# Optimization experiments

Measured on AMD Instinct MI355X. Metric: run time of the kernel, lower is better.

The kernel has to match this reference:

```python
import jax, jax.numpy as jnp
import numpy as np

N_NODES = 500_000
N_EDGES = 8_000_000
N_GRAPHS = 1000


def _mlp(x, w1, b1, w2, b2):
    # Linear -> SELU -> Linear (torch Sequential equivalent)
    return jax.nn.selu(x @ w1 + b1) @ w2 + b2


def setup_inputs() -> dict:
    key = jax.random.key(0)
    ks = jax.random.split(key, 25)
    p = lambda i, shape: jax.random.normal(ks[i], shape, jnp.float32) * 0.1
    return {
        "nodes": jax.random.normal(ks[0], (N_NODES, 1), jnp.float32),
        "edges": jax.random.normal(ks[1], (N_EDGES, 1), jnp.float32),
        "senders": jax.random.randint(ks[2], (N_EDGES,), 0, N_NODES),
        "receivers": jax.random.randint(ks[3], (N_EDGES,), 0, N_NODES),
        "graph_ids": jnp.sort(jax.random.randint(ks[4], (N_NODES,), 0, N_GRAPHS)),
        "num_graphs": N_GRAPHS,
        # permutate_nodes: 2 -> 10 -> 10
        "pn_w1": p(5, (2, 10)), "pn_b1": p(6, (10,)), "pn_w2": p(7, (10, 10)), "pn_b2": p(8, (10,)),
        # update_edges: 11 -> 5 -> 1
        "ue_w1": p(9, (11, 5)), "ue_b1": p(10, (5,)), "ue_w2": p(11, (5, 1)), "ue_b2": p(12, (1,)),
        # permutate_edges: 1 -> 5 -> 10
        "pe_w1": p(13, (1, 5)), "pe_b1": p(14, (5,)), "pe_w2": p(15, (5, 10)), "pe_b2": p(16, (10,)),
        # update_nodes: 11 -> 5 -> 1
        "un_w1": p(17, (11, 5)), "un_b1": p(18, (5,)), "un_w2": p(19, (5, 1)), "un_b2": p(20, (1,)),
        # predict: 11 -> 10 -> 10
        "pr_w1": p(21, (11, 10)), "pr_b1": p(22, (10,)), "pr_w2": p(23, (10, 10)), "pr_b2": p(24, (10,)),
    }


def reference(nodes, edges, pn_w1, pn_b1, pn_w2, pn_b2,
              ue_w1, ue_b1, ue_w2, ue_b2,
              pe_w1, pe_b1, pe_w2, pe_b2,
              un_w1, un_b1, un_w2, un_b2,
              pr_w1, pr_b1, pr_w2, pr_b2,
              senders, receivers, graph_ids, num_graphs):
    # gather node feats to edges: [recv || send] -> (E, 2)
    collected = jnp.concatenate([nodes[receivers], nodes[senders]], axis=-1)
    h1_nodes = _mlp(collected, pn_w1, pn_b1, pn_w2, pn_b2)  # (E, 10)
    h1_edges = edges  # (E, 1)
    for _ in range(3):
        h1_edges = _mlp(jnp.concatenate([h1_edges, h1_nodes], axis=-1),
                        ue_w1, ue_b1, ue_w2, ue_b2)  # (E, 1)
    # edges -> nodes aggregation (sum over receiver)
    edges_of_nodes = jax.ops.segment_sum(h1_edges, receivers, num_segments=nodes.shape[0])  # (N, 1)
    h2_edges = _mlp(edges_of_nodes, pe_w1, pe_b1, pe_w2, pe_b2)  # (N, 10)
    h2_nodes = nodes  # (N, 1)
    for _ in range(3):
        h2_nodes = _mlp(jnp.concatenate([h2_nodes, h2_edges], axis=-1),
                        un_w1, un_b1, un_w2, un_b2)  # (N, 1)
    # nodes -> globals aggregation (sum per graph)
    g = jax.ops.segment_sum(jnp.concatenate([h2_nodes, h2_edges], axis=-1),
                            graph_ids, num_segments=num_graphs)  # (G, 11)
    out = _mlp(g, pr_w1, pr_b1, pr_w2, pr_b2)  # (G, 10)
    return jax.nn.softmax(out, axis=-1)
```

## Files before the change

kernel.cpp:

```cpp
#include <hip/hip_runtime.h>
#include <hip/hip_fp16.h>
#include <math.h>

#define N_NODES_C  500000
#define N_EDGES_C  8000000
#define N_GRAPHS_C 1000
#define NGROUPS_C  (N_EDGES_C / 4)

#define BSHIFT  11
#define BWIDTH  2048
#define NBKT    245

#define PART_TPB 512
#define EPB     16384
#define GPB     (EPB / 4)
#define NPB     ((NGROUPS_C + GPB - 1) / GPB)
#define SROW    496
#define RITER   (GPB / PART_TPB)

#define GRAPH_ACC_OFF 0
#define PARTIALS_OFF  11008
#define FW_OFF        33024
#define STARTS_OFF    33280
#define PAIRS_OFF     (STARTS_OFF + 246 * SROW)
#define WS_WORDS_NEEDED (PAIRS_OFF + NPB * EPB)
#define ZERO_HEAD     33024
#define OLD_NODE_ACC_OFF 33536
#define OLD_ZERO_WORDS   (OLD_NODE_ACC_OFF + N_NODES_C)

#define LOG2E_F 1.4426950408889634f


__device__ __forceinline__ float selu2(float xl) {
    const float C1 = 0.7282901039f;
    const float C2 = 1.7580993408473766f;
    float e = __builtin_amdgcn_exp2f(xl);
    float neg = fmaf(C2, e, -C2);
    return xl > 0.0f ? C1 * xl : neg;
}

__device__ __forceinline__ float selu_f(float x) {
    const float scale = 1.0507009873554805f;
    const float sa    = 1.0507009873554805f * 1.6732632423543772f;
    float neg = sa * (__expf(x) - 1.0f);
    return x > 0.0f ? scale * x : neg;
}

__device__ __forceinline__ void atomAddF(float* p, float v) {
    __hip_atomic_fetch_add(p, v, __ATOMIC_RELAXED, __HIP_MEMORY_SCOPE_AGENT);
}

__device__ __forceinline__ void fuse_weights(
        int t,
        const float* __restrict__ pn_w1, const float* __restrict__ pn_b1,
        const float* __restrict__ pn_w2, const float* __restrict__ pn_b2,
        const float* __restrict__ ue_w1, const float* __restrict__ ue_b1,
        const float* __restrict__ ue_w2, const float* __restrict__ ue_b2,
        const float* __restrict__ pe_w1, const float* __restrict__ pe_b1,
        const float* __restrict__ pe_w2, const float* __restrict__ pe_b2,
        const float* __restrict__ un_w1, const float* __restrict__ un_b1,
        const float* __restrict__ un_w2, const float* __restrict__ un_b2,
        float* __restrict__ fw) {
    const float L = LOG2E_F;
    if (t < 20) fw[0 + t] = pn_w1[t] * L;
    if (t < 10) fw[20 + t] = pn_b1[t] * L;
    if (t < 50) {
        int j = t / 5, k = t % 5;
        float s = 0.0f;
        for (int m = 0; m < 10; ++m) s += pn_w2[j * 10 + m] * ue_w1[(1 + m) * 5 + k];
        fw[30 + t] = s * L;
    }
    if (t < 5) {
        float s = ue_b1[t];
        for (int m = 0; m < 10; ++m) s += pn_b2[m] * ue_w1[(1 + m) * 5 + t];
        fw[80 + t] = s * L;
    }
    if (t < 5)  fw[85 + t]  = ue_w1[t] * L;
    if (t < 5)  fw[90 + t]  = ue_w2[t];
    if (t == 0) fw[95]      = ue_b2[0];
    if (t < 5)  fw[96 + t]  = pe_w1[t] * L;
    if (t < 5)  fw[101 + t] = pe_b1[t] * L;
    if (t < 50) fw[106 + t] = pe_w2[t];
    if (t < 10) fw[156 + t] = pe_b2[t];
    if (t < 25) {
        int j = t / 5, k = t % 5;
        float s = 0.0f;
        for (int m = 0; m < 10; ++m) s += pe_w2[j * 10 + m] * un_w1[(1 + m) * 5 + k];
        fw[166 + t] = s * L;
    }
    if (t < 5) {
        float s = un_b1[t];
        for (int m = 0; m < 10; ++m) s += pe_b2[m] * un_w1[(1 + m) * 5 + t];
        fw[191 + t] = s * L;
    }
    if (t < 5)  fw[196 + t] = un_w1[t] * L;
    if (t < 5)  fw[201 + t] = un_w2[t];
    if (t == 0) fw[206]     = un_b2[0];
}

__global__ __launch_bounds__(256) void k_init(
        float* __restrict__ ws,
        const float* pn_w1, const float* pn_b1, const float* pn_w2, const float* pn_b2,
        const float* ue_w1, const float* ue_b1, const float* ue_w2, const float* ue_b2,
        const float* pe_w1, const float* pe_b1, const float* pe_w2, const float* pe_b2,
        const float* un_w1, const float* un_b1, const float* un_w2, const float* un_b2) {
    int i = blockIdx.x * 256 + threadIdx.x;
    if (i < ZERO_HEAD) ws[i] = 0.0f;
    if (blockIdx.x == 0)
        fuse_weights(threadIdx.x, pn_w1, pn_b1, pn_w2, pn_b2, ue_w1, ue_b1, ue_w2, ue_b2,
                     pe_w1, pe_b1, pe_w2, pe_b2, un_w1, un_b1, un_w2, un_b2, ws + FW_OFF);
}

__global__ void k_fuse(const float* pn_w1, const float* pn_b1, const float* pn_w2, const float* pn_b2,
                       const float* ue_w1, const float* ue_b1, const float* ue_w2, const float* ue_b2,
                       const float* pe_w1, const float* pe_b1, const float* pe_w2, const float* pe_b2,
                       const float* un_w1, const float* un_b1, const float* un_w2, const float* un_b2,
                       float* fw) {
    fuse_weights(threadIdx.x, pn_w1, pn_b1, pn_w2, pn_b2, ue_w1, ue_b1, ue_w2, ue_b2,
                 pe_w1, pe_b1, pe_w2, pe_b2, un_w1, un_b1, un_w2, un_b2, fw);
}

__global__ void k_final(const float* __restrict__ graph_acc,
                        const float* __restrict__ partials,
                        const float* __restrict__ pr_w1, const float* __restrict__ pr_b1,
                        const float* __restrict__ pr_w2, const float* __restrict__ pr_b2,
                        float* __restrict__ out) {
    int g = blockIdx.x * blockDim.x + threadIdx.x;
    if (g >= N_GRAPHS_C) return;
    float gv[11];
#pragma unroll
    for (int f = 0; f < 11; ++f)
        gv[f] = graph_acc[g * 11 + f] + partials[g * 11 + f] + partials[11000 + g * 11 + f];
    float h[10];
#pragma unroll
    for (int j = 0; j < 10; ++j) {
        float z = pr_b1[j];
#pragma unroll
        for (int f = 0; f < 11; ++f) z = fmaf(gv[f], pr_w1[f * 10 + j], z);
        h[j] = selu_f(z);
    }
    float o[10];
    float mx = -1e30f;
#pragma unroll
    for (int j = 0; j < 10; ++j) {
        float z = pr_b2[j];
#pragma unroll
        for (int m = 0; m < 10; ++m) z = fmaf(h[m], pr_w2[m * 10 + j], z);
        o[j] = z;
        mx = fmaxf(mx, z);
    }
    float sum = 0.0f;
#pragma unroll
    for (int j = 0; j < 10; ++j) { o[j] = __expf(o[j] - mx); sum += o[j]; }
    float inv = 1.0f / sum;
#pragma unroll
    for (int j = 0; j < 10; ++j) out[g * 10 + j] = o[j] * inv;
}


__global__ __launch_bounds__(PART_TPB, 4) void k_part(
        const float* __restrict__ nodes, const float* __restrict__ edges,
        const int* __restrict__ senders, const int* __restrict__ receivers,
        const float* __restrict__ fw, int* __restrict__ starts_T,
        unsigned int* __restrict__ pairs) {
    __shared__ int hist[256];
    __shared__ int cursorS[256];
    __shared__ unsigned int staged[EPB];

    int tid = threadIdx.x;
    int p   = blockIdx.x;
    int gstart = p * GPB;
    int gnum   = NGROUPS_C - gstart;
    if (gnum > GPB) gnum = GPB;

    float w_pn1[20], b_pn1[10], W_eb[50], b_eb[5], w1r0[5], w2e[5];
#pragma unroll
    for (int j = 0; j < 20; ++j) w_pn1[j] = fw[j];
#pragma unroll
    for (int j = 0; j < 10; ++j) b_pn1[j] = fw[20 + j];
#pragma unroll
    for (int j = 0; j < 50; ++j) W_eb[j] = fw[30 + j];
#pragma unroll
    for (int j = 0; j < 5; ++j) b_eb[j] = fw[80 + j];
#pragma unroll
    for (int j = 0; j < 5; ++j) w1r0[j] = fw[85 + j];
#pragma unroll
    for (int j = 0; j < 5; ++j) w2e[j] = fw[90 + j];
    float b2e = fw[95];

    if (tid < 256) hist[tid] = 0;
    __syncthreads();

    int4 rv4[RITER];
#pragma unroll
    for (int r = 0; r < RITER; ++r) {
        int idx = r * PART_TPB + tid;
        int gi  = gstart + (idx < gnum ? idx : 0);
        rv4[r] = ((const int4*)receivers)[gi];
        if (idx < gnum) {
            atomicAdd(&hist[rv4[r].x >> BSHIFT], 1);
            atomicAdd(&hist[rv4[r].y >> BSHIFT], 1);
            atomicAdd(&hist[rv4[r].z >> BSHIFT], 1);
            atomicAdd(&hist[rv4[r].w >> BSHIFT], 1);
        }
    }
    __syncthreads();

    int orig = 0, val = 0;
    if (tid < 256) { orig = hist[tid]; val = orig; }
    for (int d = 1; d < 256; d <<= 1) {
        int add = 0;
        if (tid >= d && tid < 256) add = hist[tid - d];
        __syncthreads();
        if (tid >= d && tid < 256) { val += add; hist[tid] = val; }
        __syncthreads();
    }
    int excl = val - orig;
    if (tid < 256) cursorS[tid] = excl;
    if (tid < 246) starts_T[tid * SROW + p] = excl;
    __syncthreads();

    float4 e4buf[2];
    int4   s4buf[2];
    float  nsb[2][4], nrb[2][4];

    {
        int gi0 = gstart + (tid < gnum ? tid : 0);
        e4buf[0] = ((const float4*)edges)[gi0];
        s4buf[0] = ((const int4*)senders)[gi0];
        nsb[0][0] = nodes[s4buf[0].x]; nsb[0][1] = nodes[s4buf[0].y];
        nsb[0][2] = nodes[s4buf[0].z]; nsb[0][3] = nodes[s4buf[0].w];
        nrb[0][0] = nodes[rv4[0].x];   nrb[0][1] = nodes[rv4[0].y];
        nrb[0][2] = nodes[rv4[0].z];   nrb[0][3] = nodes[rv4[0].w];
        int idx1 = PART_TPB + tid;
        int gi1 = gstart + (idx1 < gnum ? idx1 : 0);
        e4buf[1] = ((const float4*)edges)[gi1];
        s4buf[1] = ((const int4*)senders)[gi1];
    }

#pragma unroll
    for (int r = 0; r < RITER; ++r) {
        const int pb = r & 1;
        float ev[4] = {e4buf[pb].x, e4buf[pb].y, e4buf[pb].z, e4buf[pb].w};
        int   rv[4] = {rv4[r].x, rv4[r].y, rv4[r].z, rv4[r].w};
        float nsv[4] = {nsb[pb][0], nsb[pb][1], nsb[pb][2], nsb[pb][3]};
        float nrv[4] = {nrb[pb][0], nrb[pb][1], nrb[pb][2], nrb[pb][3]};

        if (r + 2 < RITER) {
            int idx = (r + 2) * PART_TPB + tid;
            int gi  = gstart + (idx < gnum ? idx : 0);
            e4buf[pb] = ((const float4*)edges)[gi];
            s4buf[pb] = ((const int4*)senders)[gi];
        }
        if (r + 1 < RITER) {
            const int qb = pb ^ 1;
            nsb[qb][0] = nodes[s4buf[qb].x]; nsb[qb][1] = nodes[s4buf[qb].y];
            nsb[qb][2] = nodes[s4buf[qb].z]; nsb[qb][3] = nodes[s4buf[qb].w];
            nrb[qb][0] = nodes[rv4[r + 1].x]; nrb[qb][1] = nodes[rv4[r + 1].y];
            nrb[qb][2] = nodes[rv4[r + 1].z]; nrb[qb][3] = nodes[rv4[r + 1].w];
        }

        bool validr = (r * PART_TPB + tid) < gnum;
#pragma unroll
        for (int u = 0; u < 4; ++u) {
            float nr = nrv[u], ns = nsv[u];
            float bs[5];
#pragma unroll
            for (int k = 0; k < 5; ++k) bs[k] = b_eb[k];
#pragma unroll
            for (int j = 0; j < 10; ++j) {
                float zl = fmaf(nr, w_pn1[j], fmaf(ns, w_pn1[10 + j], b_pn1[j]));
                float sz = selu2(zl);
#pragma unroll
                for (int k = 0; k < 5; ++k) bs[k] = fmaf(sz, W_eb[j * 5 + k], bs[k]);
            }
            float e = ev[u];
#pragma unroll
            for (int it = 0; it < 3; ++it) {
                float acc2 = b2e;
#pragma unroll
                for (int k = 0; k < 5; ++k) {
                    float tt = selu2(fmaf(e, w1r0[k], bs[k]));
                    acc2 = fmaf(tt, w2e[k], acc2);
                }
                e = acc2;
            }
            if (validr) {
                int bkt  = rv[u] >> BSHIFT;
                int slot = atomicAdd(&cursorS[bkt], 1);
                unsigned int pk = ((unsigned int)(rv[u] & (BWIDTH - 1)) << 16)
                                | (unsigned int)__half_as_ushort(__float2half_rn(e));
                staged[slot] = pk;
            }
        }
    }
    __syncthreads();

    const uint4* staged4 = (const uint4*)staged;
    uint4* dst = (uint4*)(pairs + (size_t)p * EPB);
    for (int i = tid; i < gnum; i += PART_TPB) dst[i] = staged4[i];
}

__global__ __launch_bounds__(1024) void k_gather(
        const float* __restrict__ nodes, const int* __restrict__ graph_ids,
        const float* __restrict__ fw, const int* __restrict__ starts_T,
        const unsigned int* __restrict__ pairs, float* __restrict__ graph_acc,
        float* __restrict__ partials) {
    __shared__ float accf[BWIDTH];
    __shared__ int s0[SROW], s1[SROW];
    __shared__ float garr[32 * 11];
    int tid = threadIdx.x;
    int b   = blockIdx.x;

    accf[tid] = 0.0f; accf[1024 + tid] = 0.0f;
    if (tid < 352) garr[tid] = 0.0f;
    for (int i = tid; i < NPB; i += 1024) {
        s0[i] = starts_T[b * SROW + i];
        s1[i] = starts_T[(b + 1) * SROW + i];
    }
    __syncthreads();

    int g32 = tid >> 5, lane = tid & 31;
    for (int p = g32; p < NPB; p += 32) {
        int st = s0[p], en = s1[p];
        const unsigned int* seg = pairs + (size_t)p * EPB + st;
        int cnt = en - st;
        for (int i = lane; i < cnt; i += 32) {
            unsigned int pk = seg[i];
            atomicAdd(&accf[(pk >> 16) & (BWIDTH - 1)],
                      __half2float(__ushort_as_half((unsigned short)(pk & 0xffff))));
        }
    }
    __syncthreads();

    float w_pe1[5], b_pe1[5], pe_w2[50], pe_b2[10], W_nb[25], b_nb[5], w1r0n[5], w2n[5];
#pragma unroll
    for (int j = 0; j < 5; ++j) w_pe1[j] = fw[96 + j];
#pragma unroll
    for (int j = 0; j < 5; ++j) b_pe1[j] = fw[101 + j];
#pragma unroll
    for (int j = 0; j < 50; ++j) pe_w2[j] = fw[106 + j];
#pragma unroll
    for (int j = 0; j < 10; ++j) pe_b2[j] = fw[156 + j];
#pragma unroll
    for (int j = 0; j < 25; ++j) W_nb[j] = fw[166 + j];
#pragma unroll
    for (int j = 0; j < 5; ++j) b_nb[j] = fw[191 + j];
#pragma unroll
    for (int j = 0; j < 5; ++j) w1r0n[j] = fw[196 + j];
#pragma unroll
    for (int j = 0; j < 5; ++j) w2n[j] = fw[201 + j];
    float b2n = fw[206];

    int nodeBase = b << BSHIFT;
    int lastIdx  = nodeBase + BWIDTH;
    if (lastIdx > N_NODES_C) lastIdx = N_NODES_C;
    int gidBase = graph_ids[nodeBase];
    int gidEnd  = graph_ids[lastIdx - 1];

#pragma unroll
    for (int q = 0; q < 2; ++q) {
        int local = q * 1024 + tid;
        int i = nodeBase + local;
        bool valid = i < N_NODES_C;

        float s = accf[local];
        float t5[5];
#pragma unroll
        for (int k = 0; k < 5; ++k) t5[k] = selu2(fmaf(s, w_pe1[k], b_pe1[k]));
        float he[10];
#pragma unroll
        for (int m = 0; m < 10; ++m) {
            float a = pe_b2[m];
#pragma unroll
            for (int k = 0; k < 5; ++k) a = fmaf(t5[k], pe_w2[k * 10 + m], a);
            he[m] = a;
        }
        float bs[5];
#pragma unroll
        for (int k = 0; k < 5; ++k) {
            float a = b_nb[k];
#pragma unroll
            for (int t = 0; t < 5; ++t) a = fmaf(t5[t], W_nb[t * 5 + k], a);
            bs[k] = a;
        }
        float n = valid ? nodes[i] : 0.0f;
#pragma unroll
        for (int it = 0; it < 3; ++it) {
            float a = b2n;
#pragma unroll
            for (int k = 0; k < 5; ++k) {
                float tt = selu2(fmaf(n, w1r0n[k], bs[k]));
                a = fmaf(tt, w2n[k], a);
            }
            n = a;
        }

        int gid = valid ? graph_ids[i] : -1;
        if (!valid) {
            n = 0.0f;
#pragma unroll
            for (int m = 0; m < 10; ++m) he[m] = 0.0f;
        }

        int gid0 = __shfl(gid, 0, 64);
        bool allsame = __all(gid == gid0) && (gid0 >= 0);
        if (allsame) {
            float v = n;
#pragma unroll
            for (int off = 32; off > 0; off >>= 1) v += __shfl_down(v, off, 64);
            float vh[10];
#pragma unroll
            for (int m = 0; m < 10; ++m) {
                float ww = he[m];
#pragma unroll
                for (int off = 32; off > 0; off >>= 1) ww += __shfl_down(ww, off, 64);
                vh[m] = ww;
            }
            if ((tid & 63) == 0) {
                int off = gid0 - gidBase;
                if (off >= 0 && off < 32) {
                    atomicAdd(&garr[off * 11 + 0], v);
#pragma unroll
                    for (int m = 0; m < 10; ++m) atomicAdd(&garr[off * 11 + 1 + m], vh[m]);
                } else {
                    atomAddF(&graph_acc[gid0 * 11 + 0], v);
#pragma unroll
                    for (int m = 0; m < 10; ++m) atomAddF(&graph_acc[gid0 * 11 + 1 + m], vh[m]);
                }
            }
        } else if (valid) {
            int off = gid - gidBase;
            if (off >= 0 && off < 32) {
                atomicAdd(&garr[off * 11 + 0], n);
#pragma unroll
                for (int m = 0; m < 10; ++m) atomicAdd(&garr[off * 11 + 1 + m], he[m]);
            } else {
                atomAddF(&graph_acc[gid * 11 + 0], n);
#pragma unroll
                for (int m = 0; m < 10; ++m) atomAddF(&graph_acc[gid * 11 + 1 + m], he[m]);
            }
        }
    }
    __syncthreads();

    int ngl = gidEnd - gidBase + 1;
    if (ngl > 32) ngl = 32;
    int par = (b & 1) * 11000;
    for (int t = tid; t < ngl * 11; t += 1024) {
        int off = t / 11, f = t - off * 11;
        partials[par + (gidBase + off) * 11 + f] = garr[t];
    }
}


__global__ __launch_bounds__(256) void k_zero(float* __restrict__ ws, int len4) {
    int i = blockIdx.x * 256 + threadIdx.x;
    if (i < len4) ((float4*)ws)[i] = make_float4(0.f, 0.f, 0.f, 0.f);
}

__global__ __launch_bounds__(256) void k_edges(
        const float* __restrict__ nodes, const float* __restrict__ edges,
        const int* __restrict__ senders, const int* __restrict__ receivers,
        const float* __restrict__ fw, float* __restrict__ node_acc) {
    float w_pn1[20], b_pn1[10], W_eb[50], b_eb[5], w1r0[5], w2e[5];
#pragma unroll
    for (int j = 0; j < 20; ++j) w_pn1[j] = fw[j];
#pragma unroll
    for (int j = 0; j < 10; ++j) b_pn1[j] = fw[20 + j];
#pragma unroll
    for (int j = 0; j < 50; ++j) W_eb[j] = fw[30 + j];
#pragma unroll
    for (int j = 0; j < 5; ++j) b_eb[j] = fw[80 + j];
#pragma unroll
    for (int j = 0; j < 5; ++j) w1r0[j] = fw[85 + j];
#pragma unroll
    for (int j = 0; j < 5; ++j) w2e[j] = fw[90 + j];
    float b2e = fw[95];

    int g = blockIdx.x * 256 + threadIdx.x;
    if (g >= NGROUPS_C) return;

    float4 e4 = ((const float4*)edges)[g];
    int4  s4 = ((const int4*)senders)[g];
    int4  r4 = ((const int4*)receivers)[g];
    float ev[4] = {e4.x, e4.y, e4.z, e4.w};
    int   sv[4] = {s4.x, s4.y, s4.z, s4.w};
    int   rv[4] = {r4.x, r4.y, r4.z, r4.w};
    float nsv[4], nrv[4];
#pragma unroll
    for (int u = 0; u < 4; ++u) { nsv[u] = nodes[sv[u]]; nrv[u] = nodes[rv[u]]; }
#pragma unroll
    for (int u = 0; u < 4; ++u) {
        float nr = nrv[u], ns = nsv[u];
        float bs[5];
#pragma unroll
        for (int k = 0; k < 5; ++k) bs[k] = b_eb[k];
#pragma unroll
        for (int j = 0; j < 10; ++j) {
            float zl = fmaf(nr, w_pn1[j], fmaf(ns, w_pn1[10 + j], b_pn1[j]));
            float sz = selu2(zl);
#pragma unroll
            for (int k = 0; k < 5; ++k) bs[k] = fmaf(sz, W_eb[j * 5 + k], bs[k]);
        }
        float e = ev[u];
#pragma unroll
        for (int it = 0; it < 3; ++it) {
            float acc2 = b2e;
#pragma unroll
            for (int k = 0; k < 5; ++k) {
                float tt = selu2(fmaf(e, w1r0[k], bs[k]));
                acc2 = fmaf(tt, w2e[k], acc2);
            }
            e = acc2;
        }
        atomAddF(&node_acc[rv[u]], e);
    }
}

__global__ __launch_bounds__(256) void k_nodes(
        const float* __restrict__ nodes, const int* __restrict__ graph_ids,
        const float* __restrict__ fw, const float* __restrict__ node_acc,
        float* __restrict__ graph_acc) {
    float w_pe1[5], b_pe1[5], pe_w2[50], pe_b2[10], W_nb[25], b_nb[5], w1r0n[5], w2n[5];
#pragma unroll
    for (int j = 0; j < 5; ++j) w_pe1[j] = fw[96 + j];
#pragma unroll
    for (int j = 0; j < 5; ++j) b_pe1[j] = fw[101 + j];
#pragma unroll
    for (int j = 0; j < 50; ++j) pe_w2[j] = fw[106 + j];
#pragma unroll
    for (int j = 0; j < 10; ++j) pe_b2[j] = fw[156 + j];
#pragma unroll
    for (int j = 0; j < 25; ++j) W_nb[j] = fw[166 + j];
#pragma unroll
    for (int j = 0; j < 5; ++j) b_nb[j] = fw[191 + j];
#pragma unroll
    for (int j = 0; j < 5; ++j) w1r0n[j] = fw[196 + j];
#pragma unroll
    for (int j = 0; j < 5; ++j) w2n[j] = fw[201 + j];
    float b2n = fw[206];

    int i = blockIdx.x * 256 + threadIdx.x;
    bool valid = i < N_NODES_C;
    int ii = valid ? i : (N_NODES_C - 1);

    float s = node_acc[ii];
    float t5[5];
#pragma unroll
    for (int k = 0; k < 5; ++k) t5[k] = selu2(fmaf(s, w_pe1[k], b_pe1[k]));
    float he[10];
#pragma unroll
    for (int m = 0; m < 10; ++m) {
        float a = pe_b2[m];
#pragma unroll
        for (int k = 0; k < 5; ++k) a = fmaf(t5[k], pe_w2[k * 10 + m], a);
        he[m] = a;
    }
    float bs[5];
#pragma unroll
    for (int k = 0; k < 5; ++k) {
        float a = b_nb[k];
#pragma unroll
        for (int t = 0; t < 5; ++t) a = fmaf(t5[t], W_nb[t * 5 + k], a);
        bs[k] = a;
    }
    float n = nodes[ii];
#pragma unroll
    for (int it = 0; it < 3; ++it) {
        float a = b2n;
#pragma unroll
        for (int k = 0; k < 5; ++k) {
            float tt = selu2(fmaf(n, w1r0n[k], bs[k]));
            a = fmaf(tt, w2n[k], a);
        }
        n = a;
    }

    int gid = valid ? graph_ids[ii] : -1;
    if (!valid) {
        n = 0.0f;
#pragma unroll
        for (int m = 0; m < 10; ++m) he[m] = 0.0f;
    }

    int gid0 = __shfl(gid, 0, 64);
    bool allsame = __all(gid == gid0) && (gid0 >= 0);
    if (allsame) {
        float v = n;
#pragma unroll
        for (int off = 32; off > 0; off >>= 1) v += __shfl_down(v, off, 64);
        float vh[10];
#pragma unroll
        for (int m = 0; m < 10; ++m) {
            float ww = he[m];
#pragma unroll
            for (int off = 32; off > 0; off >>= 1) ww += __shfl_down(ww, off, 64);
            vh[m] = ww;
        }
        if ((threadIdx.x & 63) == 0) {
            atomAddF(&graph_acc[gid0 * 11 + 0], v);
#pragma unroll
            for (int m = 0; m < 10; ++m) atomAddF(&graph_acc[gid0 * 11 + 1 + m], vh[m]);
        }
    } else if (valid) {
        atomAddF(&graph_acc[gid * 11 + 0], n);
#pragma unroll
        for (int m = 0; m < 10; ++m) atomAddF(&graph_acc[gid * 11 + 1 + m], he[m]);
    }
}


extern "C" void kernel_launch(void* const* d_in, const int* in_sizes, int n_in,
                              void* d_out, int out_size, void* d_ws, size_t ws_size,
                              hipStream_t stream) {
    const float* nodes     = (const float*)d_in[0];
    const float* edges     = (const float*)d_in[1];
    const int*   senders   = (const int*)d_in[2];
    const int*   receivers = (const int*)d_in[3];
    const int*   graph_ids = (const int*)d_in[4];
    const float* pn_w1 = (const float*)d_in[6];
    const float* pn_b1 = (const float*)d_in[7];
    const float* pn_w2 = (const float*)d_in[8];
    const float* pn_b2 = (const float*)d_in[9];
    const float* ue_w1 = (const float*)d_in[10];
    const float* ue_b1 = (const float*)d_in[11];
    const float* ue_w2 = (const float*)d_in[12];
    const float* ue_b2 = (const float*)d_in[13];
    const float* pe_w1 = (const float*)d_in[14];
    const float* pe_b1 = (const float*)d_in[15];
    const float* pe_w2 = (const float*)d_in[16];
    const float* pe_b2 = (const float*)d_in[17];
    const float* un_w1 = (const float*)d_in[18];
    const float* un_b1 = (const float*)d_in[19];
    const float* un_w2 = (const float*)d_in[20];
    const float* un_b2 = (const float*)d_in[21];
    const float* pr_w1 = (const float*)d_in[22];
    const float* pr_b1 = (const float*)d_in[23];
    const float* pr_w2 = (const float*)d_in[24];
    const float* pr_b2 = (const float*)d_in[25];

    float* ws        = (float*)d_ws;
    float* graph_acc = ws + GRAPH_ACC_OFF;
    float* partials  = ws + PARTIALS_OFF;
    float* fw        = ws + FW_OFF;
    float* outp      = (float*)d_out;

    if (ws_size >= (size_t)WS_WORDS_NEEDED * 4) {
        int* starts_T        = (int*)ws + STARTS_OFF;
        unsigned int* pairs  = (unsigned int*)ws + PAIRS_OFF;

        hipLaunchKernelGGL(k_init, dim3((ZERO_HEAD + 255) / 256), dim3(256), 0, stream, ws,
                           pn_w1, pn_b1, pn_w2, pn_b2, ue_w1, ue_b1, ue_w2, ue_b2,
                           pe_w1, pe_b1, pe_w2, pe_b2, un_w1, un_b1, un_w2, un_b2);
        hipLaunchKernelGGL(k_part, dim3(NPB), dim3(PART_TPB), 0, stream,
                           nodes, edges, senders, receivers, fw, starts_T, pairs);
        hipLaunchKernelGGL(k_gather, dim3(NBKT), dim3(1024), 0, stream,
                           nodes, graph_ids, fw, starts_T, pairs, graph_acc, partials);
        hipLaunchKernelGGL(k_final, dim3((N_GRAPHS_C + 255) / 256), dim3(256), 0, stream,
                           graph_acc, partials, pr_w1, pr_b1, pr_w2, pr_b2, outp);
    } else {
        float* node_acc = ws + OLD_NODE_ACC_OFF;
        int len4 = OLD_ZERO_WORDS / 4;
        hipLaunchKernelGGL(k_zero, dim3((len4 + 255) / 256), dim3(256), 0, stream, ws, len4);
        hipLaunchKernelGGL(k_fuse, dim3(1), dim3(64), 0, stream,
                           pn_w1, pn_b1, pn_w2, pn_b2, ue_w1, ue_b1, ue_w2, ue_b2,
                           pe_w1, pe_b1, pe_w2, pe_b2, un_w1, un_b1, un_w2, un_b2, fw);
        hipLaunchKernelGGL(k_edges, dim3((NGROUPS_C + 255) / 256), dim3(256), 0, stream,
                           nodes, edges, senders, receivers, fw, node_acc);
        hipLaunchKernelGGL(k_nodes, dim3((N_NODES_C + 255) / 256), dim3(256), 0, stream,
                           nodes, graph_ids, fw, node_acc, graph_acc);
        hipLaunchKernelGGL(k_final, dim3((N_GRAPHS_C + 255) / 256), dim3(256), 0, stream,
                           graph_acc, partials, pr_w1, pr_b1, pr_w2, pr_b2, outp);
    }
}
```

Measured before the change: 321.5 us.

## Move edge MLP into bucketed gather kernel and merge init into partition

The partition kernel no longer computes the edge MLP. It packs the local receiver index, sender index and raw edge value into 64-bit records, bucketed by receiver, and also takes over zeroing and weight fusion so the separate init launch is removed. The gather kernel does a binary search over per-partition prefix counts to spread work evenly, computes the edge MLP with receiver features taken from shared memory, and accumulates in shared memory. This removes one launch and the fp16 rounding of edge results, and uses smaller partitions. In exchange the staged traffic doubles (64-bit records instead of 32-bit), the random sender gathers move into the gather kernel, and the fused weights are written by block 0 of the same kernel that the next kernel reads.

After: 300.4 us. 1.07x faster.

```diff
diff --git a/kernel.cpp b/kernel.cpp
--- a/kernel.cpp
+++ b/kernel.cpp
@@ -11,20 +11,22 @@
 #define BWIDTH  2048
 #define NBKT    245
 
-#define PART_TPB 512
-#define EPB     16384
-#define GPB     (EPB / 4)
-#define NPB     ((NGROUPS_C + GPB - 1) / GPB)
-#define SROW    496
-#define RITER   (GPB / PART_TPB)
+#define P2_TPB  512
+#define EPB2    8192
+#define GPB2    (EPB2 / 4)
+#define NPB2    ((NGROUPS_C + GPB2 - 1) / GPB2)
+#define SROW2   992
+#define RITER2  (GPB2 / P2_TPB)
 
 #define GRAPH_ACC_OFF 0
 #define PARTIALS_OFF  11008
 #define FW_OFF        33024
-#define STARTS_OFF    33280
-#define PAIRS_OFF     (STARTS_OFF + 246 * SROW)
-#define WS_WORDS_NEEDED (PAIRS_OFF + NPB * EPB)
 #define ZERO_HEAD     33024
+
+#define STARTS2_OFF   33280
+#define PAIRS64_OFF   (STARTS2_OFF + 246 * SROW2)
+#define WS2_WORDS_NEEDED (PAIRS64_OFF + NPB2 * EPB2 * 2)
+
 #define OLD_NODE_ACC_OFF 33536
 #define OLD_ZERO_WORDS   (OLD_NODE_ACC_OFF + N_NODES_C)
 
@@ -98,19 +100,6 @@
     if (t == 0) fw[206]     = un_b2[0];
 }
 
-__global__ __launch_bounds__(256) void k_init(
-        float* __restrict__ ws,
-        const float* pn_w1, const float* pn_b1, const float* pn_w2, const float* pn_b2,
-        const float* ue_w1, const float* ue_b1, const float* ue_w2, const float* ue_b2,
-        const float* pe_w1, const float* pe_b1, const float* pe_w2, const float* pe_b2,
-        const float* un_w1, const float* un_b1, const float* un_w2, const float* un_b2) {
-    int i = blockIdx.x * 256 + threadIdx.x;
-    if (i < ZERO_HEAD) ws[i] = 0.0f;
-    if (blockIdx.x == 0)
-        fuse_weights(threadIdx.x, pn_w1, pn_b1, pn_w2, pn_b2, ue_w1, ue_b1, ue_w2, ue_b2,
-                     pe_w1, pe_b1, pe_w2, pe_b2, un_w1, un_b1, un_w2, un_b2, ws + FW_OFF);
-}
-
 __global__ void k_fuse(const float* pn_w1, const float* pn_b1, const float* pn_w2, const float* pn_b2,
                        const float* ue_w1, const float* ue_b1, const float* ue_w2, const float* ue_b2,
                        const float* pe_w1, const float* pe_b1, const float* pe_w2, const float* pe_b2,
@@ -158,43 +147,41 @@
 }
 
 
-__global__ __launch_bounds__(PART_TPB, 4) void k_part(
-        const float* __restrict__ nodes, const float* __restrict__ edges,
+__global__ __launch_bounds__(P2_TPB) void k_part2(
+        float* __restrict__ ws,
+        const float* __restrict__ edges,
         const int* __restrict__ senders, const int* __restrict__ receivers,
-        const float* __restrict__ fw, int* __restrict__ starts_T,
-        unsigned int* __restrict__ pairs) {
+        int* __restrict__ starts_T, unsigned long long* __restrict__ pairs64,
+        const float* pn_w1, const float* pn_b1, const float* pn_w2, const float* pn_b2,
+        const float* ue_w1, const float* ue_b1, const float* ue_w2, const float* ue_b2,
+        const float* pe_w1, const float* pe_b1, const float* pe_w2, const float* pe_b2,
+        const float* un_w1, const float* un_b1, const float* un_w2, const float* un_b2) {
     __shared__ int hist[256];
     __shared__ int cursorS[256];
-    __shared__ unsigned int staged[EPB];
+    __shared__ alignas(16) unsigned long long staged[EPB2];
 
     int tid = threadIdx.x;
     int p   = blockIdx.x;
-    int gstart = p * GPB;
+
+    if (tid < 34) {
+        int z = p * 34 + tid;
+        if (z < ZERO_HEAD) ws[z] = 0.0f;
+    }
+    if (p == 0)
+        fuse_weights(tid, pn_w1, pn_b1, pn_w2, pn_b2, ue_w1, ue_b1, ue_w2, ue_b2,
+                     pe_w1, pe_b1, pe_w2, pe_b2, un_w1, un_b1, un_w2, un_b2, ws + FW_OFF);
+
+    int gstart = p * GPB2;
     int gnum   = NGROUPS_C - gstart;
-    if (gnum > GPB) gnum = GPB;
-
-    float w_pn1[20], b_pn1[10], W_eb[50], b_eb[5], w1r0[5], w2e[5];
-#pragma unroll
-    for (int j = 0; j < 20; ++j) w_pn1[j] = fw[j];
-#pragma unroll
-    for (int j = 0; j < 10; ++j) b_pn1[j] = fw[20 + j];
-#pragma unroll
-    for (int j = 0; j < 50; ++j) W_eb[j] = fw[30 + j];
-#pragma unroll
-    for (int j = 0; j < 5; ++j) b_eb[j] = fw[80 + j];
-#pragma unroll
-    for (int j = 0; j < 5; ++j) w1r0[j] = fw[85 + j];
-#pragma unroll
-    for (int j = 0; j < 5; ++j) w2e[j] = fw[90 + j];
-    float b2e = fw[95];
+    if (gnum > GPB2) gnum = GPB2;
 
     if (tid < 256) hist[tid] = 0;
     __syncthreads();
 
-    int4 rv4[RITER];
-#pragma unroll
-    for (int r = 0; r < RITER; ++r) {
-        int idx = r * PART_TPB + tid;
+    int4 rv4[RITER2];
+#pragma unroll
+    for (int r = 0; r < RITER2; ++r) {
+        int idx = r * P2_TPB + tid;
         int gi  = gstart + (idx < gnum ? idx : 0);
         rv4[r] = ((const int4*)receivers)[gi];
         if (idx < gnum) {
@@ -217,53 +204,176 @@
     }
     int excl = val - orig;
     if (tid < 256) cursorS[tid] = excl;
-    if (tid < 246) starts_T[tid * SROW + p] = excl;
+    if (tid < 246) starts_T[tid * SROW2 + p] = excl;
     __syncthreads();
 
-    float4 e4buf[2];
-    int4   s4buf[2];
-    float  nsb[2][4], nrb[2][4];
+#pragma unroll
+    for (int r = 0; r < RITER2; ++r) {
+        int idx = r * P2_TPB + tid;
+        int gi  = gstart + (idx < gnum ? idx : 0);
+        float4 e4 = ((const float4*)edges)[gi];
+        int4   s4 = ((const int4*)senders)[gi];
+        int4   rv = rv4[r];
+        if (idx < gnum) {
+            int   rvv[4] = {rv.x, rv.y, rv.z, rv.w};
+            int   svv[4] = {s4.x, s4.y, s4.z, s4.w};
+            float evv[4] = {e4.x, e4.y, e4.z, e4.w};
+#pragma unroll
+            for (int u = 0; u < 4; ++u) {
+                int bkt  = rvv[u] >> BSHIFT;
+                int slot = atomicAdd(&cursorS[bkt], 1);
+                unsigned long long pk =
+                    ((unsigned long long)(rvv[u] & (BWIDTH - 1)) << 51)
+                  | ((unsigned long long)(unsigned)svv[u] << 32)
+                  | (unsigned long long)__float_as_uint(evv[u]);
+                staged[slot] = pk;
+            }
+        }
+    }
+    __syncthreads();
+
+    const uint4* st4 = (const uint4*)staged;
+    uint4* dst = (uint4*)(pairs64 + (size_t)p * EPB2);
+    int n4 = gnum * 2;
+    for (int i = tid; i < n4; i += P2_TPB) dst[i] = st4[i];
+}
+
+__global__ __launch_bounds__(1024) void k_gather2(
+        const float* __restrict__ nodes, const int* __restrict__ graph_ids,
+        const float* __restrict__ fw, const int* __restrict__ starts_T,
+        const unsigned long long* __restrict__ pairs64,
+        float* __restrict__ graph_acc, float* __restrict__ partials) {
+    __shared__ float accf[BWIDTH];
+    __shared__ float nf[BWIDTH];
+    __shared__ int   s0[NPB2];
+    __shared__ int   pst[NPB2 + 1];
+    __shared__ int   sc[1024];
+    __shared__ float garr[32 * 11];
+    int tid = threadIdx.x;
+    int b   = blockIdx.x;
+
+    int nodeBase = b << BSHIFT;
+    int lastIdx  = nodeBase + BWIDTH;
+    if (lastIdx > N_NODES_C) lastIdx = N_NODES_C;
+    int lim = lastIdx - nodeBase;
+
+    accf[tid] = 0.0f; accf[1024 + tid] = 0.0f;
+    nf[tid]        = (tid        < lim) ? nodes[nodeBase + tid]        : 0.0f;
+    nf[1024 + tid] = (1024 + tid < lim) ? nodes[nodeBase + 1024 + tid] : 0.0f;
+    if (tid < 352) garr[tid] = 0.0f;
+
+    int cntv = 0;
+    if (tid < NPB2) {
+        int a = starts_T[b * SROW2 + tid];
+        int c = starts_T[(b + 1) * SROW2 + tid];
+        s0[tid] = a;
+        cntv = c - a;
+    }
+    sc[tid] = cntv;
+    __syncthreads();
+
+    int v = cntv;
+    for (int d = 1; d < 1024; d <<= 1) {
+        int add = (tid >= d) ? sc[tid - d] : 0;
+        __syncthreads();
+        if (tid >= d) { v += add; sc[tid] = v; }
+        __syncthreads();
+    }
+    if (tid == 0) pst[0] = 0;
+    if (tid < NPB2) pst[tid + 1] = v;
+    __syncthreads();
+
+    int M = pst[NPB2];
 
     {
-        int gi0 = gstart + (tid < gnum ? tid : 0);
-        e4buf[0] = ((const float4*)edges)[gi0];
-        s4buf[0] = ((const int4*)senders)[gi0];
-        nsb[0][0] = nodes[s4buf[0].x]; nsb[0][1] = nodes[s4buf[0].y];
-        nsb[0][2] = nodes[s4buf[0].z]; nsb[0][3] = nodes[s4buf[0].w];
-        nrb[0][0] = nodes[rv4[0].x];   nrb[0][1] = nodes[rv4[0].y];
-        nrb[0][2] = nodes[rv4[0].z];   nrb[0][3] = nodes[rv4[0].w];
-        int idx1 = PART_TPB + tid;
-        int gi1 = gstart + (idx1 < gnum ? idx1 : 0);
-        e4buf[1] = ((const float4*)edges)[gi1];
-        s4buf[1] = ((const int4*)senders)[gi1];
-    }
-
-#pragma unroll
-    for (int r = 0; r < RITER; ++r) {
-        const int pb = r & 1;
-        float ev[4] = {e4buf[pb].x, e4buf[pb].y, e4buf[pb].z, e4buf[pb].w};
-        int   rv[4] = {rv4[r].x, rv4[r].y, rv4[r].z, rv4[r].w};
-        float nsv[4] = {nsb[pb][0], nsb[pb][1], nsb[pb][2], nsb[pb][3]};
-        float nrv[4] = {nrb[pb][0], nrb[pb][1], nrb[pb][2], nrb[pb][3]};
-
-        if (r + 2 < RITER) {
-            int idx = (r + 2) * PART_TPB + tid;
-            int gi  = gstart + (idx < gnum ? idx : 0);
-            e4buf[pb] = ((const float4*)edges)[gi];
-            s4buf[pb] = ((const int4*)senders)[gi];
-        }
-        if (r + 1 < RITER) {
-            const int qb = pb ^ 1;
-            nsb[qb][0] = nodes[s4buf[qb].x]; nsb[qb][1] = nodes[s4buf[qb].y];
-            nsb[qb][2] = nodes[s4buf[qb].z]; nsb[qb][3] = nodes[s4buf[qb].w];
-            nrb[qb][0] = nodes[rv4[r + 1].x]; nrb[qb][1] = nodes[rv4[r + 1].y];
-            nrb[qb][2] = nodes[rv4[r + 1].z]; nrb[qb][3] = nodes[rv4[r + 1].w];
-        }
-
-        bool validr = (r * PART_TPB + tid) < gnum;
-#pragma unroll
-        for (int u = 0; u < 4; ++u) {
-            float nr = nrv[u], ns = nsv[u];
+        float w_pn1[20], b_pn1[10], W_eb[50], b_eb[5], w1r0[5], w2e[5];
+#pragma unroll
+        for (int j = 0; j < 20; ++j) w_pn1[j] = fw[j];
+#pragma unroll
+        for (int j = 0; j < 10; ++j) b_pn1[j] = fw[20 + j];
+#pragma unroll
+        for (int j = 0; j < 50; ++j) W_eb[j] = fw[30 + j];
+#pragma unroll
+        for (int j = 0; j < 5; ++j) b_eb[j] = fw[80 + j];
+#pragma unroll
+        for (int j = 0; j < 5; ++j) w1r0[j] = fw[85 + j];
+#pragma unroll
+        for (int j = 0; j < 5; ++j) w2e[j] = fw[90 + j];
+        float b2e = fw[95];
+
+        int i = tid;
+#pragma unroll 1
+        for (; i + 1024 < M; i += 2048) {
+            int iA = i, iB = i + 1024;
+            int loA = 0, hiA = NPB2, loB = 0, hiB = NPB2;
+#pragma unroll
+            for (int s = 0; s < 10; ++s) {
+                int mA = (loA + hiA) >> 1;
+                int mB = (loB + hiB) >> 1;
+                int pA = pst[mA];
+                int pB = pst[mB];
+                if (pA <= iA) loA = mA; else hiA = mA;
+                if (pB <= iB) loB = mB; else hiB = mB;
+            }
+            unsigned long long pkA =
+                pairs64[(size_t)loA * EPB2 + s0[loA] + (iA - pst[loA])];
+            unsigned long long pkB =
+                pairs64[(size_t)loB * EPB2 + s0[loB] + (iB - pst[loB])];
+            float nsA = nodes[(int)((pkA >> 32) & 0x7FFFFULL)];
+            float nsB = nodes[(int)((pkB >> 32) & 0x7FFFFULL)];
+            int   rlA = (int)(pkA >> 51);
+            int   rlB = (int)(pkB >> 51);
+            float nrA = nf[rlA];
+            float nrB = nf[rlB];
+            float eA  = __uint_as_float((unsigned)pkA);
+            float eB  = __uint_as_float((unsigned)pkB);
+
+            float bsA[5], bsB[5];
+#pragma unroll
+            for (int k = 0; k < 5; ++k) { bsA[k] = b_eb[k]; bsB[k] = b_eb[k]; }
+#pragma unroll
+            for (int j = 0; j < 10; ++j) {
+                float zlA = fmaf(nrA, w_pn1[j], fmaf(nsA, w_pn1[10 + j], b_pn1[j]));
+                float zlB = fmaf(nrB, w_pn1[j], fmaf(nsB, w_pn1[10 + j], b_pn1[j]));
+                float szA = selu2(zlA);
+                float szB = selu2(zlB);
+#pragma unroll
+                for (int k = 0; k < 5; ++k) {
+                    bsA[k] = fmaf(szA, W_eb[j * 5 + k], bsA[k]);
+                    bsB[k] = fmaf(szB, W_eb[j * 5 + k], bsB[k]);
+                }
+            }
+#pragma unroll
+            for (int it = 0; it < 3; ++it) {
+                float aA = b2e, aB = b2e;
+#pragma unroll
+                for (int k = 0; k < 5; ++k) {
+                    float tA = selu2(fmaf(eA, w1r0[k], bsA[k]));
+                    float tB = selu2(fmaf(eB, w1r0[k], bsB[k]));
+                    aA = fmaf(tA, w2e[k], aA);
+                    aB = fmaf(tB, w2e[k], aB);
+                }
+                eA = aA; eB = aB;
+            }
+            atomicAdd(&accf[rlA], eA);
+            atomicAdd(&accf[rlB], eB);
+        }
+#pragma unroll 1
+        for (; i < M; i += 1024) {
+            int lo = 0, hi = NPB2;
+#pragma unroll
+            for (int s = 0; s < 10; ++s) {
+                int mid = (lo + hi) >> 1;
+                if (pst[mid] <= i) lo = mid; else hi = mid;
+            }
+            unsigned long long pk =
+                pairs64[(size_t)lo * EPB2 + s0[lo] + (i - pst[lo])];
+            int   rl   = (int)(pk >> 51);
+            int   sidx = (int)((pk >> 32) & 0x7FFFFULL);
+            float e    = __uint_as_float((unsigned)pk);
+            float nr   = nf[rl];
+            float ns   = nodes[sidx];
+
             float bs[5];
 #pragma unroll
             for (int k = 0; k < 5; ++k) bs[k] = b_eb[k];
@@ -274,7 +384,6 @@
 #pragma unroll
                 for (int k = 0; k < 5; ++k) bs[k] = fmaf(sz, W_eb[j * 5 + k], bs[k]);
             }
-            float e = ev[u];
 #pragma unroll
             for (int it = 0; it < 3; ++it) {
                 float acc2 = b2e;
@@ -285,50 +394,7 @@
                 }
                 e = acc2;
             }
-            if (validr) {
-                int bkt  = rv[u] >> BSHIFT;
-                int slot = atomicAdd(&cursorS[bkt], 1);
-                unsigned int pk = ((unsigned int)(rv[u] & (BWIDTH - 1)) << 16)
-                                | (unsigned int)__half_as_ushort(__float2half_rn(e));
-                staged[slot] = pk;
-            }
-        }
-    }
-    __syncthreads();
-
-    const uint4* staged4 = (const uint4*)staged;
-    uint4* dst = (uint4*)(pairs + (size_t)p * EPB);
-    for (int i = tid; i < gnum; i += PART_TPB) dst[i] = staged4[i];
-}
-
-__global__ __launch_bounds__(1024) void k_gather(
-        const float* __restrict__ nodes, const int* __restrict__ graph_ids,
-        const float* __restrict__ fw, const int* __restrict__ starts_T,
-        const unsigned int* __restrict__ pairs, float* __restrict__ graph_acc,
-        float* __restrict__ partials) {
-    __shared__ float accf[BWIDTH];
-    __shared__ int s0[SROW], s1[SROW];
-    __shared__ float garr[32 * 11];
-    int tid = threadIdx.x;
-    int b   = blockIdx.x;
-
-    accf[tid] = 0.0f; accf[1024 + tid] = 0.0f;
-    if (tid < 352) garr[tid] = 0.0f;
-    for (int i = tid; i < NPB; i += 1024) {
-        s0[i] = starts_T[b * SROW + i];
-        s1[i] = starts_T[(b + 1) * SROW + i];
-    }
-    __syncthreads();
-
-    int g32 = tid >> 5, lane = tid & 31;
-    for (int p = g32; p < NPB; p += 32) {
-        int st = s0[p], en = s1[p];
-        const unsigned int* seg = pairs + (size_t)p * EPB + st;
-        int cnt = en - st;
-        for (int i = lane; i < cnt; i += 32) {
-            unsigned int pk = seg[i];
-            atomicAdd(&accf[(pk >> 16) & (BWIDTH - 1)],
-                      __half2float(__ushort_as_half((unsigned short)(pk & 0xffff))));
+            atomicAdd(&accf[rl], e);
         }
     }
     __syncthreads();
@@ -352,9 +418,6 @@
     for (int j = 0; j < 5; ++j) w2n[j] = fw[201 + j];
     float b2n = fw[206];
 
-    int nodeBase = b << BSHIFT;
-    int lastIdx  = nodeBase + BWIDTH;
-    if (lastIdx > N_NODES_C) lastIdx = N_NODES_C;
     int gidBase = graph_ids[nodeBase];
     int gidEnd  = graph_ids[lastIdx - 1];
 
@@ -384,7 +447,7 @@
             for (int t = 0; t < 5; ++t) a = fmaf(t5[t], W_nb[t * 5 + k], a);
             bs[k] = a;
         }
-        float n = valid ? nodes[i] : 0.0f;
+        float n = valid ? nf[local] : 0.0f;
 #pragma unroll
         for (int it = 0; it < 3; ++it) {
             float a = b2n;
@@ -406,9 +469,9 @@
         int gid0 = __shfl(gid, 0, 64);
         bool allsame = __all(gid == gid0) && (gid0 >= 0);
         if (allsame) {
-            float v = n;
-#pragma unroll
-            for (int off = 32; off > 0; off >>= 1) v += __shfl_down(v, off, 64);
+            float vv = n;
+#pragma unroll
+            for (int off = 32; off > 0; off >>= 1) vv += __shfl_down(vv, off, 64);
             float vh[10];
 #pragma unroll
             for (int m = 0; m < 10; ++m) {
@@ -420,11 +483,11 @@
             if ((tid & 63) == 0) {
                 int off = gid0 - gidBase;
                 if (off >= 0 && off < 32) {
-                    atomicAdd(&garr[off * 11 + 0], v);
+                    atomicAdd(&garr[off * 11 + 0], vv);
 #pragma unroll
                     for (int m = 0; m < 10; ++m) atomicAdd(&garr[off * 11 + 1 + m], vh[m]);
                 } else {
-                    atomAddF(&graph_acc[gid0 * 11 + 0], v);
+                    atomAddF(&graph_acc[gid0 * 11 + 0], vv);
 #pragma unroll
                     for (int m = 0; m < 10; ++m) atomAddF(&graph_acc[gid0 * 11 + 1 + m], vh[m]);
                 }
@@ -646,17 +709,16 @@
     float* fw        = ws + FW_OFF;
     float* outp      = (float*)d_out;
 
-    if (ws_size >= (size_t)WS_WORDS_NEEDED * 4) {
-        int* starts_T        = (int*)ws + STARTS_OFF;
-        unsigned int* pairs  = (unsigned int*)ws + PAIRS_OFF;
-
-        hipLaunchKernelGGL(k_init, dim3((ZERO_HEAD + 255) / 256), dim3(256), 0, stream, ws,
+    if (ws_size >= (size_t)WS2_WORDS_NEEDED * 4) {
+        int* starts_T = (int*)ws + STARTS2_OFF;
+        unsigned long long* pairs64 = (unsigned long long*)((int*)ws + PAIRS64_OFF);
+
+        hipLaunchKernelGGL(k_part2, dim3(NPB2), dim3(P2_TPB), 0, stream,
+                           ws, edges, senders, receivers, starts_T, pairs64,
                            pn_w1, pn_b1, pn_w2, pn_b2, ue_w1, ue_b1, ue_w2, ue_b2,
                            pe_w1, pe_b1, pe_w2, pe_b2, un_w1, un_b1, un_w2, un_b2);
-        hipLaunchKernelGGL(k_part, dim3(NPB), dim3(PART_TPB), 0, stream,
-                           nodes, edges, senders, receivers, fw, starts_T, pairs);
-        hipLaunchKernelGGL(k_gather, dim3(NBKT), dim3(1024), 0, stream,
-                           nodes, graph_ids, fw, starts_T, pairs, graph_acc, partials);
+        hipLaunchKernelGGL(k_gather2, dim3(NBKT), dim3(1024), 0, stream,
+                           nodes, graph_ids, fw, starts_T, pairs64, graph_acc, partials);
         hipLaunchKernelGGL(k_final, dim3((N_GRAPHS_C + 255) / 256), dim3(256), 0, stream,
                            graph_acc, partials, pr_w1, pr_b1, pr_w2, pr_b2, outp);
     } else {
```
